# Kernel optimization log

Hardware: AMD Instinct MI355X
Metric: run time of the kernel (lower is better)

## Reference

```python
import jax, jax.numpy as jnp
import numpy as np

T, B, IN, H, OUT = 512, 256, 8, 512, 5


def setup_inputs() -> dict:
    key = jax.random.key(0)
    ks = jax.random.split(key, 12)
    # PyTorch default init: U(-1/sqrt(H), 1/sqrt(H))
    bound = 1.0 / np.sqrt(H)
    u = lambda k, shape: jax.random.uniform(k, shape, jnp.float32, -bound, bound)
    return {
        "rnn_input": jax.random.normal(ks[0], (T, B, IN), jnp.float32),
        # GRU layer 0 (input -> H); gates stacked [r, z, n] as in torch.nn.GRUCell
        "W_ih0": u(ks[1], (3 * H, IN)),
        "W_hh0": u(ks[2], (3 * H, H)),
        "b_ih0": u(ks[3], (3 * H,)),
        "b_hh0": u(ks[4], (3 * H,)),
        # GRU layer 1 (H -> H)
        "W_ih1": u(ks[5], (3 * H, H)),
        "W_hh1": u(ks[6], (3 * H, H)),
        "b_ih1": u(ks[7], (3 * H,)),
        "b_hh1": u(ks[8], (3 * H,)),
        # Linear head H -> OUT
        "W_out": u(ks[9], (OUT, H)),
        "b_out": u(ks[10], (OUT,)),
    }


def _gru_cell(x, h, W_ih, W_hh, b_ih, b_hh):
    # torch.nn.GRUCell math, gates stacked as [r, z, n]
    gi = x @ W_ih.T + b_ih          # [B, 3H]
    gh = h @ W_hh.T + b_hh          # [B, 3H]
    i_r, i_z, i_n = jnp.split(gi, 3, axis=-1)
    h_r, h_z, h_n = jnp.split(gh, 3, axis=-1)
    r = jax.nn.sigmoid(i_r + h_r)
    z = jax.nn.sigmoid(i_z + h_z)
    n = jnp.tanh(i_n + r * h_n)
    return (1.0 - z) * n + z * h


def reference(rnn_input, W_ih0, W_hh0, b_ih0, b_hh0,
              W_ih1, W_hh1, b_ih1, b_hh1, W_out, b_out):
    Bn = rnn_input.shape[1]
    Hn = W_hh0.shape[1]
    h0 = jnp.zeros((Bn, Hn), rnn_input.dtype)
    h1 = jnp.zeros((Bn, Hn), rnn_input.dtype)

    def step(carry, x_t):
        h0, h1 = carry
        h0 = _gru_cell(x_t, h0, W_ih0, W_hh0, b_ih0, b_hh0)
        h1 = _gru_cell(h0, h1, W_ih1, W_hh1, b_ih1, b_hh1)
        return (h0, h1), None

    (h0, h1), _ = jax.lax.scan(step, (h0, h1), rnn_input)
    # module returns the linear head applied to the last hidden state
    return h1 @ W_out.T + b_out  # [B, OUT]
```

## Files before the change

kernel.cpp:

```cpp
#include <hip/hip_runtime.h>

typedef _Float16 half8 __attribute__((ext_vector_type(8)));
typedef float    f32x4 __attribute__((ext_vector_type(4)));

#define TT 512
#define BB 256
#define INDIM 8
#define HH 512


__global__ void prep_kernel(const float* __restrict__ Whh0,
                            const float* __restrict__ Wih1,
                            const float* __restrict__ Whh1,
                            float* __restrict__ ws)
{
    const int NW = 32*144*512;
    _Float16* b16 = (_Float16*)(ws + 131072);
    _Float16* Wpk = b16 + 524288;
    int* flags = (int*)((char*)ws + 6291456);
    long long idx = (long long)blockIdx.x*256 + threadIdx.x;
    if (idx < NW) {
        int e   = (int)idx;
        int c   = e / (144*512);
        int rem = e % (144*512);
        int nl  = rem >> 9;
        int k   = rem & 511;
        int g9  = nl >> 4;
        int m   = nl & 15;
        int j   = c*16 + m;
        float v;
        if      (g9 < 3) v = Whh0[(size_t)(g9*HH + j)*HH + k];
        else if (g9 < 6) v = Wih1[(size_t)((g9-3)*HH + j)*HH + k];
        else             v = Whh1[(size_t)((g9-6)*HH + j)*HH + k];
        Wpk[e] = (_Float16)v;
    } else if (idx < NW + 524288) {
        b16[idx - NW] = (_Float16)0.0f;
    } else if (idx < NW + 524288 + 512) {
        flags[idx - NW - 524288] = 0;
    } else if (idx < NW + 524288 + 512 + 131072) {
        ws[idx - (NW + 524288 + 512)] = 1.0e-3f;
    }
}

__global__ void __launch_bounds__(256, 1)
gru_main(const float* __restrict__ x,
         const float* __restrict__ Wih0, const float* __restrict__ bih0,
         const float* __restrict__ bhh0, const float* __restrict__ bih1,
         const float* __restrict__ bhh1, float* __restrict__ ws)
{
    __shared__ __align__(16) _Float16 Wl[75264];

    const int tid   = threadIdx.x;
    const int blk   = blockIdx.x;
    const int layer = blk >> 7;
    const int lblk  = blk & 127;
    const int jg    = lblk & 15;
    const int bg    = lblk >> 4;

    float* h1f = ws;
    _Float16* b16 = (_Float16*)(ws + 131072);
    _Float16* h0h[2] = { b16,          b16 + 131072 };
    _Float16* h1h[2] = { b16 + 262144, b16 + 393216 };
    const _Float16* Wpk = b16 + 524288;

    volatile int* flag0row = (volatile int*)((char*)ws + 6291456) + bg*32;
    volatile int* flag1row = (volatile int*)((char*)ws + 6291456) + 256 + bg*32;

    const int lane = tid & 63;
    const int wv   = tid >> 6;
    const int ct   = wv & 1;
    const int rt   = wv >> 1;
    const int m    = lane & 15;
    const int q    = lane >> 4;
    const int j    = jg*32 + ct*16 + m;
    const int bb   = bg*32 + rt*16;

    const _Float16* WpkB = Wpk + (size_t)(jg*2 + ct)*(144*512);

    const int pidx = lane & 15;
    const int psel = (lane >> 4) & 1;
    volatile int* pollptr = psel ? (flag1row + pidx) : (flag0row + pidx);

    if (layer == 0) {
        for (int t2 = tid; t2 < 2*48*64; t2 += 256) {
            int c = t2 / 3072, rem = t2 % 3072, nl = rem >> 6, g = rem & 63;
            *(float4*)&Wl[c*24960 + nl*520 + g*8] =
                *(const float4*)&Wpk[((size_t)(jg*2 + c)*144 + nl)*512 + g*8];
        }
        __syncthreads();
        const _Float16* WlA = Wl + ct*24960;

        float w0[3][8];
        #pragma unroll
        for (int g = 0; g < 3; ++g)
            #pragma unroll
            for (int kk = 0; kk < 8; ++kk)
                w0[g][kk] = Wih0[(size_t)(g*HH + j)*INDIM + kk];
        const float br0  = bih0[j]      + bhh0[j];
        const float bz0  = bih0[HH+j]   + bhh0[HH+j];
        const float bni0 = bih0[2*HH+j];
        const float bnh0 = bhh0[2*HH+j];

        float h0pr[4] = {0.f,0.f,0.f,0.f};

        f32x4 xA[4], xB[4];
        #pragma unroll
        for (int r = 0; r < 4; ++r) {
            const float* xv = x + (size_t)(bb + q*4 + r)*INDIM;
            asm volatile("global_load_dwordx4 %0, %1, off" : "=v"(xA[r]) : "v"(xv));
            asm volatile("global_load_dwordx4 %0, %1, off" : "=v"(xB[r]) : "v"(xv + 4));
        }

        for (int p = 0; p < TT; ++p) {
            const _Float16* a0base = h0h[(p+1)&1] + (size_t)(bb + m)*HH + q*8;
            half8 a0s[16];
            #pragma unroll
            for (int s = 0; s < 16; ++s)
                asm volatile("global_load_dwordx4 %0, %1, off sc0 sc1"
                             : "=v"(a0s[s]) : "v"(a0base + s*32));
            asm volatile("s_waitcnt vmcnt(0)"
                : "+v"(a0s[0]),"+v"(a0s[1]),"+v"(a0s[2]),"+v"(a0s[3]),
                  "+v"(a0s[4]),"+v"(a0s[5]),"+v"(a0s[6]),"+v"(a0s[7]),
                  "+v"(a0s[8]),"+v"(a0s[9]),"+v"(a0s[10]),"+v"(a0s[11]),
                  "+v"(a0s[12]),"+v"(a0s[13]),"+v"(a0s[14]),"+v"(a0s[15]));
            asm volatile(""
                : "+v"(xA[0]),"+v"(xA[1]),"+v"(xA[2]),"+v"(xA[3]),
                  "+v"(xB[0]),"+v"(xB[1]),"+v"(xB[2]),"+v"(xB[3]));

            f32x4 acc0[3];
            #pragma unroll
            for (int g = 0; g < 3; ++g) acc0[g] = (f32x4){0.f,0.f,0.f,0.f};
            #pragma unroll
            for (int s = 0; s < 16; ++s) {
                #pragma unroll
                for (int g = 0; g < 3; ++g) {
                    half8 bf = *(const half8*)&WlA[(g*16+m)*520 + (s*4+q)*8];
                    acc0[g] = __builtin_amdgcn_mfma_f32_16x16x32_f16(a0s[s], bf, acc0[g], 0, 0, 0);
                }
            }

            _Float16* h0n = h0h[p&1];
            #pragma unroll
            for (int r = 0; r < 4; ++r) {
                const int b = bb + q*4 + r;
                f32x4 xa = xA[r], xb = xB[r];
                float gr = xa[0]*w0[0][0]+xa[1]*w0[0][1]+xa[2]*w0[0][2]+xa[3]*w0[0][3]
                         + xb[0]*w0[0][4]+xb[1]*w0[0][5]+xb[2]*w0[0][6]+xb[3]*w0[0][7];
                float gz = xa[0]*w0[1][0]+xa[1]*w0[1][1]+xa[2]*w0[1][2]+xa[3]*w0[1][3]
                         + xb[0]*w0[1][4]+xb[1]*w0[1][5]+xb[2]*w0[1][6]+xb[3]*w0[1][7];
                float gn = xa[0]*w0[2][0]+xa[1]*w0[2][1]+xa[2]*w0[2][2]+xa[3]*w0[2][3]
                         + xb[0]*w0[2][4]+xb[1]*w0[2][5]+xb[2]*w0[2][6]+xb[3]*w0[2][7];
                float rg = 1.f/(1.f + __expf(-(gr + acc0[0][r] + br0)));
                float zg = 1.f/(1.f + __expf(-(gz + acc0[1][r] + bz0)));
                float ng = tanhf(gn + bni0 + rg*(acc0[2][r] + bnh0));
                float hv = (1.f - zg)*ng + zg*h0pr[r];
                h0pr[r] = hv;
                _Float16 hv16 = (_Float16)hv;
                asm volatile("global_store_short %0, %1, off sc0 sc1"
                             :: "v"(h0n + (size_t)b*HH + j), "v"(hv16) : "memory");
            }
            asm volatile("s_waitcnt vmcnt(0)" ::: "memory");
            __syncthreads();
            if (tid == 0) flag0row[jg] = p + 1;

            {
                const size_t psafe = (p + 1 < TT) ? (size_t)(p + 1) : (size_t)(TT - 1);
                #pragma unroll
                for (int r = 0; r < 4; ++r) {
                    const float* xv = x + (psafe*BB + (size_t)(bb + q*4 + r))*INDIM;
                    asm volatile("global_load_dwordx4 %0, %1, off" : "=v"(xA[r]) : "v"(xv));
                    asm volatile("global_load_dwordx4 %0, %1, off" : "=v"(xB[r]) : "v"(xv + 4));
                }
            }
            if (p < TT-1) {
                if (tid < 64) {
                    const int tgt = p + 1 - psel;
                    while (true) {
                        int v = *pollptr;
                        if (__all(v >= tgt)) break;
                        __builtin_amdgcn_s_sleep(1);
                    }
                }
                __syncthreads();
            }
        }
    } else {
        for (int t2 = tid; t2 < 2*48*64; t2 += 256) {
            int c = t2 / 3072, rem = t2 % 3072, nl = rem >> 6, g = rem & 63;
            *(float4*)&Wl[c*24960 + nl*520 + g*8] =
                *(const float4*)&Wpk[((size_t)(jg*2 + c)*144 + 96 + nl)*512 + g*8];
        }
        for (int t2 = tid; t2 < 2*48*32; t2 += 256) {
            int c = t2 / 1536, rem = t2 % 1536, nl = rem >> 5, g = rem & 31;
            *(float4*)&Wl[49920 + c*12672 + nl*264 + g*8] =
                *(const float4*)&Wpk[((size_t)(jg*2 + c)*144 + 48 + nl)*512 + g*8];
        }
        __syncthreads();
        const _Float16* WlC = Wl + ct*24960;
        const _Float16* WlB = Wl + 49920 + ct*12672;

        const float br1  = bih1[j]      + bhh1[j];
        const float bz1  = bih1[HH+j]   + bhh1[HH+j];
        const float bni1 = bih1[2*HH+j];
        const float bnh1 = bhh1[2*HH+j];

        float h1pr[4] = {0.f,0.f,0.f,0.f};

        for (int t = 0; t < TT; ++t) {
            if (tid < 64) {
                const int tgt = t + 1 - psel;
                while (true) {
                    int v = *pollptr;
                    if (__all(v >= tgt)) break;
                    __builtin_amdgcn_s_sleep(1);
                }
            }
            __syncthreads();

            const _Float16* aXbase = h0h[t&1]     + (size_t)(bb + m)*HH + q*8;
            const _Float16* a1base = h1h[(t+1)&1] + (size_t)(bb + m)*HH + q*8;
            half8 aXs[16], a1s[16];
            #pragma unroll
            for (int s = 0; s < 16; ++s) {
                asm volatile("global_load_dwordx4 %0, %1, off sc0 sc1"
                             : "=v"(aXs[s]) : "v"(aXbase + s*32));
                asm volatile("global_load_dwordx4 %0, %1, off sc0 sc1"
                             : "=v"(a1s[s]) : "v"(a1base + s*32));
            }
            asm volatile("s_waitcnt vmcnt(0)"
                : "+v"(aXs[0]),"+v"(aXs[1]),"+v"(aXs[2]),"+v"(aXs[3]),
                  "+v"(aXs[4]),"+v"(aXs[5]),"+v"(aXs[6]),"+v"(aXs[7]),
                  "+v"(aXs[8]),"+v"(aXs[9]),"+v"(aXs[10]),"+v"(aXs[11]),
                  "+v"(aXs[12]),"+v"(aXs[13]),"+v"(aXs[14]),"+v"(aXs[15]));
            asm volatile(""
                : "+v"(a1s[0]),"+v"(a1s[1]),"+v"(a1s[2]),"+v"(a1s[3]),
                  "+v"(a1s[4]),"+v"(a1s[5]),"+v"(a1s[6]),"+v"(a1s[7]),
                  "+v"(a1s[8]),"+v"(a1s[9]),"+v"(a1s[10]),"+v"(a1s[11]),
                  "+v"(a1s[12]),"+v"(a1s[13]),"+v"(a1s[14]),"+v"(a1s[15]));

            f32x4 acc[6];
            #pragma unroll
            for (int g = 0; g < 6; ++g) acc[g] = (f32x4){0.f,0.f,0.f,0.f};

            #pragma unroll
            for (int s = 0; s < 8; ++s) {
                #pragma unroll
                for (int gg = 0; gg < 3; ++gg) {
                    half8 bf = *(const half8*)&WlB[(gg*16+m)*264 + (s*4+q)*8];
                    acc[gg] = __builtin_amdgcn_mfma_f32_16x16x32_f16(aXs[s], bf, acc[gg], 0, 0, 0);
                }
            }
            half8 nb[3];
            #pragma unroll
            for (int gg = 0; gg < 3; ++gg)
                nb[gg] = *(const half8*)&WpkB[(size_t)(48 + gg*16 + m)*512 + 8*32 + q*8];
            #pragma unroll
            for (int s = 8; s < 16; ++s) {
                half8 cb[3];
                #pragma unroll
                for (int gg = 0; gg < 3; ++gg) cb[gg] = nb[gg];
                if (s < 15) {
                    #pragma unroll
                    for (int gg = 0; gg < 3; ++gg)
                        nb[gg] = *(const half8*)&WpkB[(size_t)(48 + gg*16 + m)*512 + (s+1)*32 + q*8];
                }
                #pragma unroll
                for (int gg = 0; gg < 3; ++gg)
                    acc[gg] = __builtin_amdgcn_mfma_f32_16x16x32_f16(aXs[s], cb[gg], acc[gg], 0, 0, 0);
            }
            #pragma unroll
            for (int s = 0; s < 16; ++s) {
                #pragma unroll
                for (int gg = 0; gg < 3; ++gg) {
                    half8 bf = *(const half8*)&WlC[(gg*16+m)*520 + (s*4+q)*8];
                    acc[3+gg] = __builtin_amdgcn_mfma_f32_16x16x32_f16(a1s[s], bf, acc[3+gg], 0, 0, 0);
                }
            }

            _Float16* h1n = h1h[t&1];
            #pragma unroll
            for (int r = 0; r < 4; ++r) {
                const int b = bb + q*4 + r;
                float rg = 1.f/(1.f + __expf(-(acc[0][r] + acc[3][r] + br1)));
                float zg = 1.f/(1.f + __expf(-(acc[1][r] + acc[4][r] + bz1)));
                float ng = tanhf(acc[2][r] + bni1 + rg*(acc[5][r] + bnh1));
                float hv = (1.f - zg)*ng + zg*h1pr[r];
                h1pr[r] = hv;
                _Float16 hv16 = (_Float16)hv;
                asm volatile("global_store_short %0, %1, off sc0 sc1"
                             :: "v"(h1n + (size_t)b*HH + j), "v"(hv16) : "memory");
                if (t == TT-1) h1f[(size_t)b*HH + j] = hv;
            }
            asm volatile("s_waitcnt vmcnt(0)" ::: "memory");
            __syncthreads();
            if (tid == 0) flag1row[jg] = t + 1;
        }
    }
}

__global__ void head_kernel(const float* __restrict__ ws,
                            const float* __restrict__ Wout,
                            const float* __restrict__ bout,
                            float* __restrict__ out)
{
    const float* h1 = ws;
    int b = blockIdx.x;
    int lane = threadIdx.x;
    for (int o = 0; o < 5; ++o) {
        float s = 0.f;
        for (int k = lane; k < HH; k += 64)
            s += h1[(size_t)b*HH + k] * Wout[(size_t)o*HH + k];
        for (int off = 32; off > 0; off >>= 1)
            s += __shfl_xor(s, off, 64);
        if (lane == 0) out[b*5 + o] = s + bout[o];
    }
}

extern "C" void kernel_launch(void* const* d_in, const int* in_sizes, int n_in,
                              void* d_out, int out_size, void* d_ws, size_t ws_size,
                              hipStream_t stream) {
    const float* x    = (const float*)d_in[0];
    const float* Wih0 = (const float*)d_in[1];
    const float* Whh0 = (const float*)d_in[2];
    const float* bih0 = (const float*)d_in[3];
    const float* bhh0 = (const float*)d_in[4];
    const float* Wih1 = (const float*)d_in[5];
    const float* Whh1 = (const float*)d_in[6];
    const float* bih1 = (const float*)d_in[7];
    const float* bhh1 = (const float*)d_in[8];
    const float* Wout = (const float*)d_in[9];
    const float* bout = (const float*)d_in[10];
    float* out = (float*)d_out;
    float* ws  = (float*)d_ws;

    const long long total = 32LL*144*512 + 524288 + 512 + 131072;
    int pblocks = (int)((total + 255) / 256);
    hipLaunchKernelGGL(prep_kernel, dim3(pblocks), dim3(256), 0, stream,
                       Whh0, Wih1, Whh1, ws);

    hipLaunchKernelGGL(gru_main, dim3(256), dim3(256), 0, stream,
                       x, Wih0, bih0, bhh0, bih1, bhh1, ws);

    hipLaunchKernelGGL(head_kernel, dim3(256), dim3(64), 0, stream,
                       (const float*)ws, Wout, bout, out);
}
```

Baseline: 5.408 ms.

## Replace post-poll barrier with LDS release flag and busy-wait FMA spinning

After wave 0 polls the global cross-block flags, it now publishes the step number in a shared-memory variable. The other waves spin on that variable, running dummy FMA chains, instead of meeting at __syncthreads. The intent is to cut barrier latency and, by keeping the ALUs busy, possibly hold clocks up during waits. The risks are extra power from the busy FMA work and weaker memory ordering, since the barrier that ordered wave 0's flag observation before the other waves' global loads is gone. The s_rel initialisation is also not followed by a barrier before its first use.

```diff
diff --git a/kernel.cpp b/kernel.cpp
--- a/kernel.cpp
+++ b/kernel.cpp
@@ -49,6 +49,7 @@
          const float* __restrict__ bhh1, float* __restrict__ ws)
 {
     __shared__ __align__(16) _Float16 Wl[75264];
+    volatile __shared__ int s_rel;
 
     const int tid   = threadIdx.x;
     const int blk   = blockIdx.x;
@@ -77,9 +78,13 @@
 
     const _Float16* WpkB = Wpk + (size_t)(jg*2 + ct)*(144*512);
 
+    if (tid == 0) s_rel = 0;
+
     const int pidx = lane & 15;
     const int psel = (lane >> 4) & 1;
     volatile int* pollptr = psel ? (flag1row + pidx) : (flag0row + pidx);
+
+    float spin = 1.0f;
 
     if (layer == 0) {
         for (int t2 = tid; t2 < 2*48*64; t2 += 256) {
@@ -173,15 +178,29 @@
                 }
             }
             if (p < TT-1) {
-                if (tid < 64) {
+                if (wv == 0) {
                     const int tgt = p + 1 - psel;
                     while (true) {
                         int v = *pollptr;
                         if (__all(v >= tgt)) break;
                         __builtin_amdgcn_s_sleep(1);
                     }
-                }
-                __syncthreads();
+                    if (lane == 0) s_rel = p + 1;
+                } else {
+                    const int tgt = p + 1;
+                    float u0 = spin, u1 = spin + 1.f, u2 = spin + 2.f, u3 = spin + 3.f;
+                    while (s_rel < tgt) {
+                        #pragma unroll
+                        for (int kk = 0; kk < 8; ++kk) {
+                            u0 = __builtin_fmaf(u0, 1.0000001f, 1.0e-30f);
+                            u1 = __builtin_fmaf(u1, 1.0000001f, 1.0e-30f);
+                            u2 = __builtin_fmaf(u2, 1.0000001f, 1.0e-30f);
+                            u3 = __builtin_fmaf(u3, 1.0000001f, 1.0e-30f);
+                        }
+                    }
+                    spin = u0 + u1 + u2 + u3;
+                    asm volatile("" :: "v"(spin));
+                }
             }
         }
     } else {
@@ -207,15 +226,29 @@
         float h1pr[4] = {0.f,0.f,0.f,0.f};
 
         for (int t = 0; t < TT; ++t) {
-            if (tid < 64) {
+            if (wv == 0) {
                 const int tgt = t + 1 - psel;
                 while (true) {
                     int v = *pollptr;
                     if (__all(v >= tgt)) break;
                     __builtin_amdgcn_s_sleep(1);
                 }
-            }
-            __syncthreads();
+                if (lane == 0) s_rel = t + 1;
+            } else {
+                const int tgt = t + 1;
+                float u0 = spin, u1 = spin + 1.f, u2 = spin + 2.f, u3 = spin + 3.f;
+                while (s_rel < tgt) {
+                    #pragma unroll
+                    for (int kk = 0; kk < 8; ++kk) {
+                        u0 = __builtin_fmaf(u0, 1.0000001f, 1.0e-30f);
+                        u1 = __builtin_fmaf(u1, 1.0000001f, 1.0e-30f);
+                        u2 = __builtin_fmaf(u2, 1.0000001f, 1.0e-30f);
+                        u3 = __builtin_fmaf(u3, 1.0000001f, 1.0e-30f);
+                    }
+                }
+                spin = u0 + u1 + u2 + u3;
+                asm volatile("" :: "v"(spin));
+            }
 
             const _Float16* aXbase = h0h[t&1]     + (size_t)(bb + m)*HH + q*8;
             const _Float16* a1base = h1h[(t+1)&1] + (size_t)(bb + m)*HH + q*8;
```

Result: slower. 5.524 ms (+2.1%).
